# Performance work log

Measured on AMD Instinct MI355X. Metric: run time of the kernel, lower is better.

## Reference

```python
import jax, jax.numpy as jnp
import numpy as np

D_MODEL = 1024
NUM_HEADS = 16
D_K = D_MODEL // NUM_HEADS
SCALE = float(np.sqrt(D_K))


def setup_inputs() -> dict:
    key = jax.random.key(0)
    ks = jax.random.split(key, 6)
    x = jax.random.normal(ks[0], (2, 2048, D_MODEL), dtype=jnp.float32)
    s = 1.0 / np.sqrt(D_MODEL)
    w_q = jax.random.uniform(ks[1], (D_MODEL, D_MODEL), jnp.float32, -s, s)
    w_k = jax.random.uniform(ks[2], (D_MODEL, D_MODEL), jnp.float32, -s, s)
    w_v = jax.random.uniform(ks[3], (D_MODEL, D_MODEL), jnp.float32, -s, s)
    w_o = jax.random.uniform(ks[4], (D_MODEL, D_MODEL), jnp.float32, -s, s)
    b_o = jax.random.uniform(ks[5], (D_MODEL,), jnp.float32, -s, s)
    return {"x": x, "w_q": w_q, "w_k": w_k, "w_v": w_v, "w_o": w_o, "b_o": b_o}


def reference(x, w_q, w_k, w_v, w_o, b_o):
    B, S, _ = x.shape
    # project and split heads: [B, H, S, d_k]
    def heads(w):
        return (x @ w.T).reshape(B, S, NUM_HEADS, D_K).transpose(0, 2, 1, 3)
    Q, K, V = heads(w_q), heads(w_k), heads(w_v)
    scores = jnp.einsum("bhqd,bhkd->bhqk", Q, K) / SCALE  # [B,H,S,S]
    attn = jax.nn.softmax(scores, axis=-1)
    context = jnp.einsum("bhqk,bhkd->bhqd", attn, V)
    context = context.transpose(0, 2, 1, 3).reshape(B, S, D_MODEL)
    return context @ w_o.T + b_o
```

## Files before the change

kernel.cpp:

```cpp
#include <hip/hip_runtime.h>

typedef unsigned short u16t;
typedef short bf16x8 __attribute__((ext_vector_type(8)));
typedef short bf16x4 __attribute__((ext_vector_type(4)));
typedef float f32x4 __attribute__((ext_vector_type(4)));

#define NHEADS 16
#define SEQ 2048
#define DMODEL 1024
#define HEAD_ELEMS (SEQ * 64)
#define LSTR 72
#define MATE ((size_t)2 * SEQ * DMODEL)
#define CSC 0.1803368801f
#define MB 4.0f

__device__ __forceinline__ u16t f2bf(float f) {
  union { float f; unsigned u; } v; v.f = f;
  unsigned r = v.u + 0x7FFFu + ((v.u >> 16) & 1u);
  return (u16t)(r >> 16);
}
__device__ __forceinline__ float bf2f(u16t b) {
  union { unsigned u; float f; } v; v.u = ((unsigned)b) << 16;
  return v.f;
}
__device__ __forceinline__ float sanef(float x) {
  return fminf(fmaxf(x, -16384.f), 16384.f);
}
__device__ __forceinline__ unsigned pk2(float a, float b) {
  union { float f; unsigned u; } x, y; x.f = a; y.f = b;
  return __builtin_amdgcn_perm(y.u + 0x8000u, x.u + 0x8000u, 0x07060302u);
}
__device__ __forceinline__ bf16x8 cvt8(const float* p) {
  const f32x4* q4 = (const f32x4*)p;
  f32x4 a = q4[0], b = q4[1];
  bf16x8 o;
  o[0] = (short)f2bf(a[0]); o[1] = (short)f2bf(a[1]);
  o[2] = (short)f2bf(a[2]); o[3] = (short)f2bf(a[3]);
  o[4] = (short)f2bf(b[0]); o[5] = (short)f2bf(b[1]);
  o[6] = (short)f2bf(b[2]); o[7] = (short)f2bf(b[3]);
  return o;
}

__device__ __forceinline__ void stage16(const u16t* g, u16t* l) {
  __builtin_amdgcn_global_load_lds(
      (const __attribute__((address_space(1))) unsigned int*)g,
      (__attribute__((address_space(3))) unsigned int*)l, 16, 0, 0);
}

struct ushort4a { u16t x, y, z, w; } __attribute__((aligned(8)));

__device__ __forceinline__ int detect_bf16_wave(const u16t* p) {
  int lane = threadIdx.x & 63;
  int cnt = 0;
#pragma unroll
  for (int i = 0; i < 8; ++i) {
    int ex = (p[2 * (lane * 8 + i)] >> 7) & 0xFF;
    cnt += (ex >= 100 && ex <= 140) ? 1 : 0;
  }
  cnt += __shfl_xor(cnt, 1);
  cnt += __shfl_xor(cnt, 2);
  cnt += __shfl_xor(cnt, 4);
  cnt += __shfl_xor(cnt, 8);
  cnt += __shfl_xor(cnt, 16);
  cnt += __shfl_xor(cnt, 32);
  return cnt >= 300;
}

__global__ __launch_bounds__(256) void qkv_kernel(
    const void* __restrict__ xv,
    const void* __restrict__ wqv, const void* __restrict__ wkv,
    const void* __restrict__ wvv,
    u16t* __restrict__ q_ws, u16t* __restrict__ k_ws, u16t* __restrict__ vt_ws) {
  __shared__ u16t As[128 * 32];
  __shared__ u16t Bs[128 * 32];
  const int bfm = detect_bf16_wave((const u16t*)xv);
  const int tid = threadIdx.x;
  const int bm0 = blockIdx.x * 128;
  const int bn0 = blockIdx.y * 128;
  const int z = blockIdx.z;
  const void* Wv = (z == 0) ? wqv : ((z == 1) ? wkv : wvv);
  const float scale = (z == 0) ? CSC : 1.0f;
  const int lane = tid & 63;
  const int w = tid >> 6;
  const int ln = lane & 15;
  const int quad = lane >> 4;
  const int wm = (w & 1) * 64;
  const int wn = (w >> 1) * 64;

  f32x4 acc[4][4] = {};

  for (int kt = 0; kt < 32; ++kt) {
    __syncthreads();
    if (bfm) {
      const u16t* x = (const u16t*)xv;
      const u16t* W = (const u16t*)Wv;
#pragma unroll
      for (int j = 0; j < 2; ++j) {
        int f = j * 256 + tid;
        int row = f >> 2;
        int col = (f & 3) * 8;
        stage16(x + (size_t)(bm0 + row) * DMODEL + kt * 32 + col, &As[f * 8]);
        stage16(W + (size_t)(bn0 + row) * DMODEL + kt * 32 + col, &Bs[f * 8]);
      }
    } else {
      const float* x = (const float*)xv;
      const float* W = (const float*)Wv;
#pragma unroll
      for (int j = 0; j < 2; ++j) {
        int f = j * 256 + tid;
        int row = f >> 2;
        int col = (f & 3) * 8;
        *(bf16x8*)&As[f * 8] = cvt8(x + (size_t)(bm0 + row) * DMODEL + kt * 32 + col);
        *(bf16x8*)&Bs[f * 8] = cvt8(W + (size_t)(bn0 + row) * DMODEL + kt * 32 + col);
      }
    }
    __syncthreads();
    bf16x8 a[4], b[4];
#pragma unroll
    for (int t = 0; t < 4; ++t)
      a[t] = *(const bf16x8*)&As[(wm + t * 16 + ln) * 32 + quad * 8];
#pragma unroll
    for (int t = 0; t < 4; ++t)
      b[t] = *(const bf16x8*)&Bs[(wn + t * 16 + ln) * 32 + quad * 8];
#pragma unroll
    for (int i = 0; i < 4; ++i)
#pragma unroll
      for (int jn = 0; jn < 4; ++jn)
        acc[i][jn] = __builtin_amdgcn_mfma_f32_16x16x32_bf16(a[i], b[jn], acc[i][jn], 0, 0, 0);
  }

#pragma unroll
  for (int i = 0; i < 4; ++i) {
    int m_base = bm0 + wm + i * 16 + quad * 4;
#pragma unroll
    for (int jn = 0; jn < 4; ++jn) {
      int n = bn0 + wn + jn * 16 + ln;
      int h = n >> 6, dk = n & 63;
      if (z < 2) {
        u16t* dst = (z == 0) ? q_ws : k_ws;
#pragma unroll
        for (int r = 0; r < 4; ++r) {
          int m = m_base + r;
          int bb = m >> 11, s = m & 2047;
          dst[(size_t)(bb * NHEADS + h) * HEAD_ELEMS + s * 64 + dk] =
              f2bf(sanef(acc[i][jn][r]) * scale);
        }
      } else {
        int bb = m_base >> 11, s = m_base & 2047;
        ushort4a pk;
        pk.x = f2bf(sanef(acc[i][jn][0]));
        pk.y = f2bf(sanef(acc[i][jn][1]));
        pk.z = f2bf(sanef(acc[i][jn][2]));
        pk.w = f2bf(sanef(acc[i][jn][3]));
        *(ushort4a*)&vt_ws[(size_t)(bb * NHEADS + h) * HEAD_ELEMS + (size_t)dk * SEQ + s] = pk;
      }
    }
  }
}

__global__ __launch_bounds__(512, 4) void attn_kernel(
    const u16t* __restrict__ q_ws, const u16t* __restrict__ k_ws,
    const u16t* __restrict__ vt_ws, u16t* __restrict__ ctx_ws) {
  __shared__ u16t Ks[64 * LSTR];
  __shared__ u16t Vt[64 * LSTR];
  const int tid = threadIdx.x;
  const int w = tid >> 6;
  const int lane = tid & 63;
  const int ln = lane & 15;
  const int quad = lane >> 4;
  const int bh = blockIdx.y;
  const size_t base = (size_t)bh * HEAD_ELEMS;
  const int q0w = blockIdx.x * 128 + w * 16;

  bf16x8 aq[2];
#pragma unroll
  for (int ks = 0; ks < 2; ++ks)
    aq[ks] = *(const bf16x8*)(q_ws + base + (size_t)(q0w + ln) * 64 + ks * 32 + quad * 8);

  const int r = tid >> 3;
  const int cc = (tid & 7) * 8;
  const u16t* kp = k_ws + base + (size_t)tid * 8;
  const u16t* vp = vt_ws + base + (size_t)r * SEQ + cc;
  u16t* kl = &Ks[r * LSTR + cc];
  u16t* vl = &Vt[r * LSTR + cc];

  f32x4 accO[4] = {};
  float psum = 0.f;

  for (int kt = 0; kt < 32; ++kt) {
    bf16x8 rk = *(const bf16x8*)kp; kp += 4096;
    bf16x8 rv = *(const bf16x8*)vp; vp += 64;
    __syncthreads();
    *(bf16x8*)kl = rk;
    *(bf16x8*)vl = rv;
    __syncthreads();

    f32x4 st[4];
#pragma unroll
    for (int nt = 0; nt < 4; ++nt) {
      st[nt][0] = -MB; st[nt][1] = -MB; st[nt][2] = -MB; st[nt][3] = -MB;
    }
#pragma unroll
    for (int nt = 0; nt < 4; ++nt)
#pragma unroll
      for (int ks = 0; ks < 2; ++ks) {
        bf16x8 bk = *(const bf16x8*)&Ks[(nt * 16 + ln) * LSTR + ks * 32 + quad * 8];
        st[nt] = __builtin_amdgcn_mfma_f32_16x16x32_bf16(bk, aq[ks], st[nt], 0, 0, 0);
      }

#pragma unroll
    for (int pp = 0; pp < 2; ++pp) {
      float pv[8];
#pragma unroll
      for (int j = 0; j < 4; ++j) {
        pv[j]     = exp2f(st[2 * pp][j]);
        pv[4 + j] = exp2f(st[2 * pp + 1][j]);
      }
      psum += ((pv[0] + pv[1]) + (pv[2] + pv[3])) + ((pv[4] + pv[5]) + (pv[6] + pv[7]));
      union { unsigned u[4]; bf16x8 v; } ap;
      ap.u[0] = pk2(pv[0], pv[1]);
      ap.u[1] = pk2(pv[2], pv[3]);
      ap.u[2] = pk2(pv[4], pv[5]);
      ap.u[3] = pk2(pv[6], pv[7]);
#pragma unroll
      for (int dt = 0; dt < 4; ++dt) {
        const u16t* vrow = &Vt[(dt * 16 + ln) * LSTR + quad * 4];
        bf16x4 lo = *(const bf16x4*)(vrow + (2 * pp) * 16);
        bf16x4 hi = *(const bf16x4*)(vrow + (2 * pp + 1) * 16);
        bf16x8 bb = __builtin_shufflevector(lo, hi, 0, 1, 2, 3, 4, 5, 6, 7);
        accO[dt] = __builtin_amdgcn_mfma_f32_16x16x32_bf16(ap.v, bb, accO[dt], 0, 0, 0);
      }
    }
  }

  psum += __shfl_xor(psum, 16);
  psum += __shfl_xor(psum, 32);
  float inv[4];
#pragma unroll
  for (int rr = 0; rr < 4; ++rr) {
    float lq = __shfl(psum, quad * 4 + rr);
    inv[rr] = 1.0f / fmaxf(lq, 1e-20f);
  }
#pragma unroll
  for (int dt = 0; dt < 4; ++dt)
#pragma unroll
    for (int rr = 0; rr < 4; ++rr)
      ctx_ws[base + (size_t)(q0w + quad * 4 + rr) * 64 + dt * 16 + ln] =
          f2bf(accO[dt][rr] * inv[rr]);
}

__global__ __launch_bounds__(256, 4) void outproj_kernel(
    const u16t* __restrict__ ctx, const void* __restrict__ wov,
    const void* __restrict__ bov_, void* __restrict__ outv) {
  __shared__ u16t As[2][64 * LSTR];
  __shared__ u16t Bs[2][64 * LSTR];
  const int bfm = detect_bf16_wave((const u16t*)wov);
  const int tid = threadIdx.x;
  const int bm0 = blockIdx.x * 64;
  const int bn0 = blockIdx.y * 64;
  const int lane = tid & 63;
  const int w = tid >> 6;
  const int ln = lane & 15;
  const int quad = lane >> 4;
  const int wm = (w & 1) * 32;
  const int wn = (w >> 1) * 32;

  f32x4 acc[2][2] = {};

  auto do_mfma = [&](int cur) {
    bf16x8 a[2][2], b[2][2];
#pragma unroll
    for (int t = 0; t < 2; ++t)
#pragma unroll
      for (int ks = 0; ks < 2; ++ks) {
        a[t][ks] = *(const bf16x8*)&As[cur][(wm + t * 16 + ln) * LSTR + ks * 32 + quad * 8];
        b[t][ks] = *(const bf16x8*)&Bs[cur][(wn + t * 16 + ln) * LSTR + ks * 32 + quad * 8];
      }
#pragma unroll
    for (int p = 0; p < 2; ++p)
#pragma unroll
      for (int q = 0; q < 2; ++q)
#pragma unroll
        for (int ks = 0; ks < 2; ++ks)
          acc[p][q] = __builtin_amdgcn_mfma_f32_16x16x32_bf16(a[p][ks], b[q][ks], acc[p][q], 0, 0, 0);
  };

  const int c0 = tid, c1 = tid + 256;
  const int r0 = c0 >> 3, o0 = (c0 & 7) * 8;
  const int r1 = c1 >> 3, o1 = (c1 & 7) * 8;
  const int d0 = r0 * LSTR + o0, d1 = r1 * LSTR + o1;
  const int m0 = bm0 + r0, m1 = bm0 + r1;
  const u16t* ap0 = ctx + (size_t)((m0 >> 11) * NHEADS) * HEAD_ELEMS + (m0 & 2047) * 64 + o0;
  const u16t* ap1 = ctx + (size_t)((m1 >> 11) * NHEADS) * HEAD_ELEMS + (m1 & 2047) * 64 + o1;

  if (bfm) {
    const u16t* wo = (const u16t*)wov;
    const u16t* bp0 = wo + (size_t)(bn0 + r0) * DMODEL + o0;
    const u16t* bp1 = wo + (size_t)(bn0 + r1) * DMODEL + o1;
    bf16x8 ra0 = *(const bf16x8*)ap0, ra1 = *(const bf16x8*)ap1;
    bf16x8 rb0 = *(const bf16x8*)bp0, rb1 = *(const bf16x8*)bp1;
    *(bf16x8*)&As[0][d0] = ra0; *(bf16x8*)&As[0][d1] = ra1;
    *(bf16x8*)&Bs[0][d0] = rb0; *(bf16x8*)&Bs[0][d1] = rb1;
    __syncthreads();
    for (int kt = 0; kt < 16; ++kt) {
      int cur = kt & 1;
      if (kt < 15) {
        ap0 += HEAD_ELEMS; ap1 += HEAD_ELEMS;
        bp0 += 64; bp1 += 64;
        ra0 = *(const bf16x8*)ap0; ra1 = *(const bf16x8*)ap1;
        rb0 = *(const bf16x8*)bp0; rb1 = *(const bf16x8*)bp1;
      }
      do_mfma(cur);
      if (kt < 15) {
        int nxt = cur ^ 1;
        *(bf16x8*)&As[nxt][d0] = ra0; *(bf16x8*)&As[nxt][d1] = ra1;
        *(bf16x8*)&Bs[nxt][d0] = rb0; *(bf16x8*)&Bs[nxt][d1] = rb1;
        __syncthreads();
      }
    }
  } else {
    const float* wo = (const float*)wov;
    for (int kt = 0; kt < 16; ++kt) {
      __syncthreads();
      *(bf16x8*)&As[0][d0] = *(const bf16x8*)(ap0 + (size_t)kt * HEAD_ELEMS);
      *(bf16x8*)&As[0][d1] = *(const bf16x8*)(ap1 + (size_t)kt * HEAD_ELEMS);
      *(bf16x8*)&Bs[0][d0] = cvt8(wo + (size_t)(bn0 + r0) * DMODEL + kt * 64 + o0);
      *(bf16x8*)&Bs[0][d1] = cvt8(wo + (size_t)(bn0 + r1) * DMODEL + kt * 64 + o1);
      __syncthreads();
      do_mfma(0);
    }
  }

#pragma unroll
  for (int p = 0; p < 2; ++p) {
    int m_base = bm0 + wm + p * 16 + quad * 4;
#pragma unroll
    for (int q = 0; q < 2; ++q) {
      int n = bn0 + wn + q * 16 + ln;
      float bov = bfm ? bf2f(((const u16t*)bov_)[n]) : ((const float*)bov_)[n];
#pragma unroll
      for (int r = 0; r < 2 * 2; ++r) {
        int m = m_base + r;
        float v = sanef(acc[p][q][r] + bov);
        if (bfm) ((u16t*)outv)[(size_t)m * DMODEL + n] = f2bf(v);
        else     ((float*)outv)[(size_t)m * DMODEL + n] = v;
      }
    }
  }
}

extern "C" void kernel_launch(void* const* d_in, const int* in_sizes, int n_in,
                              void* d_out, int out_size, void* d_ws, size_t ws_size,
                              hipStream_t stream) {
  (void)in_sizes; (void)n_in; (void)out_size; (void)ws_size;
  const void* x  = d_in[0];
  const void* wq = d_in[1];
  const void* wk = d_in[2];
  const void* wv = d_in[3];
  const void* wo = d_in[4];
  const void* bo = d_in[5];

  u16t* q_ws  = (u16t*)d_ws;
  u16t* k_ws  = q_ws + MATE;
  u16t* vt_ws = k_ws + MATE;
  u16t* ctx_ws = q_ws;

  dim3 gA(32, 8, 3);
  qkv_kernel<<<gA, 256, 0, stream>>>(x, wq, wk, wv, q_ws, k_ws, vt_ws);

  dim3 gB(16, 32);
  attn_kernel<<<gB, 512, 0, stream>>>(q_ws, k_ws, vt_ws, ctx_ws);

  dim3 gC(64, 16);
  outproj_kernel<<<gC, 256, 0, stream>>>(ctx_ws, wo, bo, d_out);
}
```

Baseline: 212.4 us.

## Double-buffer K/V tiles in attention and compute row sums via MFMA

The attention kernel now double-buffers K and V tiles in LDS. The next tile's global loads are issued before the current tile's compute and written to the alternate buffer afterward, so the loop needs one barrier per iteration instead of two. The softmax denominator is now accumulated with an extra MFMA against a vector of bf16 ones, replacing the scalar adds and cross-lane shuffles. The row sum is therefore taken over the same bf16-rounded probabilities used for P·V. Probability packing switches to the hardware v_cvt_pk_bf16_f32 instruction in place of the manual perm-based rounding. Costs are doubled LDS use and extra live registers for the prefetched tile.

```diff
diff --git a/kernel.cpp b/kernel.cpp
--- a/kernel.cpp
+++ b/kernel.cpp
@@ -29,6 +29,11 @@
 __device__ __forceinline__ unsigned pk2(float a, float b) {
   union { float f; unsigned u; } x, y; x.f = a; y.f = b;
   return __builtin_amdgcn_perm(y.u + 0x8000u, x.u + 0x8000u, 0x07060302u);
+}
+__device__ __forceinline__ unsigned cvtpk2(float a, float b) {
+  unsigned r;
+  asm("v_cvt_pk_bf16_f32 %0, %1, %2" : "=v"(r) : "v"(a), "v"(b));
+  return r;
 }
 __device__ __forceinline__ bf16x8 cvt8(const float* p) {
   const f32x4* q4 = (const f32x4*)p;
@@ -161,8 +166,8 @@
 __global__ __launch_bounds__(512, 4) void attn_kernel(
     const u16t* __restrict__ q_ws, const u16t* __restrict__ k_ws,
     const u16t* __restrict__ vt_ws, u16t* __restrict__ ctx_ws) {
-  __shared__ u16t Ks[64 * LSTR];
-  __shared__ u16t Vt[64 * LSTR];
+  __shared__ u16t Ks[2][64 * LSTR];
+  __shared__ u16t Vt[2][64 * LSTR];
   const int tid = threadIdx.x;
   const int w = tid >> 6;
   const int lane = tid & 63;
@@ -177,23 +182,38 @@
   for (int ks = 0; ks < 2; ++ks)
     aq[ks] = *(const bf16x8*)(q_ws + base + (size_t)(q0w + ln) * 64 + ks * 32 + quad * 8);
 
+  bf16x8 vone;
+#pragma unroll
+  for (int i = 0; i < 8; ++i) vone[i] = (short)0x3F80;
+
   const int r = tid >> 3;
   const int cc = (tid & 7) * 8;
   const u16t* kp = k_ws + base + (size_t)tid * 8;
   const u16t* vp = vt_ws + base + (size_t)r * SEQ + cc;
-  u16t* kl = &Ks[r * LSTR + cc];
-  u16t* vl = &Vt[r * LSTR + cc];
+  const int dl = r * LSTR + cc;
 
   f32x4 accO[4] = {};
-  float psum = 0.f;
+  f32x4 accL = {};
+
+  {
+    bf16x8 rk = *(const bf16x8*)kp;
+    bf16x8 rv = *(const bf16x8*)vp;
+    *(bf16x8*)&Ks[0][dl] = rk;
+    *(bf16x8*)&Vt[0][dl] = rv;
+  }
+  __syncthreads();
 
   for (int kt = 0; kt < 32; ++kt) {
-    bf16x8 rk = *(const bf16x8*)kp; kp += 4096;
-    bf16x8 rv = *(const bf16x8*)vp; vp += 64;
-    __syncthreads();
-    *(bf16x8*)kl = rk;
-    *(bf16x8*)vl = rv;
-    __syncthreads();
+    const int cur = kt & 1;
+    bf16x8 rk, rv;
+    if (kt < 31) {
+      kp += 4096;
+      vp += 64;
+      rk = *(const bf16x8*)kp;
+      rv = *(const bf16x8*)vp;
+    }
+    const u16t* Kc = Ks[cur];
+    const u16t* Vc = Vt[cur];
 
     f32x4 st[4];
 #pragma unroll
@@ -204,7 +224,7 @@
     for (int nt = 0; nt < 4; ++nt)
 #pragma unroll
       for (int ks = 0; ks < 2; ++ks) {
-        bf16x8 bk = *(const bf16x8*)&Ks[(nt * 16 + ln) * LSTR + ks * 32 + quad * 8];
+        bf16x8 bk = *(const bf16x8*)&Kc[(nt * 16 + ln) * LSTR + ks * 32 + quad * 8];
         st[nt] = __builtin_amdgcn_mfma_f32_16x16x32_bf16(bk, aq[ks], st[nt], 0, 0, 0);
       }
 
@@ -216,31 +236,33 @@
         pv[j]     = exp2f(st[2 * pp][j]);
         pv[4 + j] = exp2f(st[2 * pp + 1][j]);
       }
-      psum += ((pv[0] + pv[1]) + (pv[2] + pv[3])) + ((pv[4] + pv[5]) + (pv[6] + pv[7]));
       union { unsigned u[4]; bf16x8 v; } ap;
-      ap.u[0] = pk2(pv[0], pv[1]);
-      ap.u[1] = pk2(pv[2], pv[3]);
-      ap.u[2] = pk2(pv[4], pv[5]);
-      ap.u[3] = pk2(pv[6], pv[7]);
+      ap.u[0] = cvtpk2(pv[0], pv[1]);
+      ap.u[1] = cvtpk2(pv[2], pv[3]);
+      ap.u[2] = cvtpk2(pv[4], pv[5]);
+      ap.u[3] = cvtpk2(pv[6], pv[7]);
+      accL = __builtin_amdgcn_mfma_f32_16x16x32_bf16(ap.v, vone, accL, 0, 0, 0);
 #pragma unroll
       for (int dt = 0; dt < 4; ++dt) {
-        const u16t* vrow = &Vt[(dt * 16 + ln) * LSTR + quad * 4];
+        const u16t* vrow = &Vc[(dt * 16 + ln) * LSTR + quad * 4];
         bf16x4 lo = *(const bf16x4*)(vrow + (2 * pp) * 16);
         bf16x4 hi = *(const bf16x4*)(vrow + (2 * pp + 1) * 16);
         bf16x8 bb = __builtin_shufflevector(lo, hi, 0, 1, 2, 3, 4, 5, 6, 7);
         accO[dt] = __builtin_amdgcn_mfma_f32_16x16x32_bf16(ap.v, bb, accO[dt], 0, 0, 0);
       }
     }
-  }
-
-  psum += __shfl_xor(psum, 16);
-  psum += __shfl_xor(psum, 32);
+
+    if (kt < 31) {
+      *(bf16x8*)&Ks[cur ^ 1][dl] = rk;
+      *(bf16x8*)&Vt[cur ^ 1][dl] = rv;
+      __syncthreads();
+    }
+  }
+
   float inv[4];
 #pragma unroll
-  for (int rr = 0; rr < 4; ++rr) {
-    float lq = __shfl(psum, quad * 4 + rr);
-    inv[rr] = 1.0f / fmaxf(lq, 1e-20f);
-  }
+  for (int rr = 0; rr < 4; ++rr)
+    inv[rr] = 1.0f / fmaxf(accL[rr], 1e-20f);
 #pragma unroll
   for (int dt = 0; dt < 4; ++dt)
 #pragma unroll
```

After: 213.2 us. Within noise of the previous version (+0.4%).
